# Performance work log

Hardware: AMD Instinct MI355X
Metric: run time of the kernel (lower is better)

Reference implementation:

```python
import jax, jax.numpy as jnp
import numpy as np

T, D, I, E, K = 256, 2048, 5632, 8, 2
P = (I * D + 4) // 5  # TQ1_0: 5 ternary values per byte
_MULT = (1, 3, 9, 27, 81)


def _unpack_tq10(packed, out_dim, in_dim):
    # packed: int32 [P], each value is a base-3 byte encoding 5 ternary digits
    digits = jnp.stack([(packed // m) % 3 for m in _MULT], axis=1)  # [P,5]
    w = digits.reshape(-1)[: out_dim * in_dim] - 1  # {-1,0,+1}
    return w.reshape(out_dim, in_dim).astype(jnp.float32)


def _tmm(x, w_packed, s, out_dim, in_dim):
    # ternary_matmul_direct: dequant ternary weight, per-output-row scale
    w = _unpack_tq10(w_packed, out_dim, in_dim)  # [out,in]
    return (x @ w.T) * s.reshape(1, -1)


def setup_inputs() -> dict:
    key = jax.random.key(0)
    ks = jax.random.split(key, 16)
    inp = {}
    inp["x"] = jax.random.normal(ks[0], (T, D), jnp.float32)
    inp["router_w"] = jax.random.normal(ks[1], (E, D), jnp.float32) * 0.02
    inp["gate_packed"] = jax.random.randint(ks[2], (E, P), 0, 243, jnp.int32)
    inp["up_packed"] = jax.random.randint(ks[3], (E, P), 0, 243, jnp.int32)
    inp["down_packed"] = jax.random.randint(ks[4], (E, P), 0, 243, jnp.int32)
    inp["gate_s"] = jax.random.uniform(ks[5], (E, I, 1), jnp.float32, 0.01, 0.05)
    inp["up_s"] = jax.random.uniform(ks[6], (E, I, 1), jnp.float32, 0.01, 0.05)
    inp["down_s"] = jax.random.uniform(ks[7], (E, D, 1), jnp.float32, 0.01, 0.05)
    inp["sh_gate_w"] = jax.random.randint(ks[8], (I, D), -127, 128, jnp.int32)
    inp["sh_up_w"] = jax.random.randint(ks[9], (I, D), -127, 128, jnp.int32)
    inp["sh_down_w"] = jax.random.randint(ks[10], (D, I), -127, 128, jnp.int32)
    inp["sh_gate_s"] = jax.random.uniform(ks[11], (I, 1), jnp.float32, 0.005, 0.02)
    inp["sh_up_s"] = jax.random.uniform(ks[12], (I, 1), jnp.float32, 0.005, 0.02)
    inp["sh_down_s"] = jax.random.uniform(ks[13], (D, 1), jnp.float32, 0.005, 0.02)
    return inp


def reference(x, router_w, gate_packed, up_packed, down_packed,
              gate_s, up_s, down_s,
              sh_gate_w, sh_up_w, sh_down_w,
              sh_gate_s, sh_up_s, sh_down_s):
    n_tok = x.shape[0]
    # ---- router: top-k + softmax over selected logits -> dense gate matrix [T,E]
    logits = x @ router_w.T
    topv, topi = jax.lax.top_k(logits, K)
    probs = jax.nn.softmax(topv, axis=-1)
    gates = jnp.zeros((n_tok, E), x.dtype).at[jnp.arange(n_tok)[:, None], topi].add(probs)
    # ---- shared INT8 SwiGLU expert (dequant matmul, per-row fp scale)
    g = jax.nn.silu((x @ sh_gate_w.T.astype(jnp.float32)) * sh_gate_s.reshape(1, -1))
    u = (x @ sh_up_w.T.astype(jnp.float32)) * sh_up_s.reshape(1, -1)
    out = ((g * u) @ sh_down_w.T.astype(jnp.float32)) * sh_down_s.reshape(1, -1)
    # ---- routed ternary TQ1_0 experts (unpack -> dequant -> SwiGLU)
    for e in range(E):
        ge = jax.nn.silu(_tmm(x, gate_packed[e], gate_s[e], I, D))
        ue = _tmm(x, up_packed[e], up_s[e], I, D)
        ye = _tmm(ge * ue, down_packed[e], down_s[e], D, I)
        out = out + gates[:, e:e + 1] * ye
    return out
```

## Files before the change

kernel.cpp:

```cpp
#include <hip/hip_runtime.h>
#include <hip/hip_bf16.h>
#include <stdint.h>

#define TT 256
#define DD 2048
#define II 5632
#define EE 8
#define PP 2306868

typedef __attribute__((ext_vector_type(8))) short bf16x8;
typedef __attribute__((ext_vector_type(4))) float f32x4;
typedef unsigned int uint;

__device__ __forceinline__ ushort f2b_rne(float f) {
  __hip_bfloat16 h = __float2bfloat16(f);
  return __builtin_bit_cast(ushort, h);
}

__device__ __forceinline__ uint pk_bf16(float lo, float hi) {
  uint r;
  asm("v_cvt_pk_bf16_f32 %0, %1, %2" : "=v"(r) : "v"(lo), "v"(hi));
  return r;
}

__device__ __forceinline__ bf16x8 ld_a(const ushort* p) {
  uint4 v = *(const uint4*)p;
  return __builtin_bit_cast(bf16x8, v);
}

__device__ __forceinline__ bf16x8 tern_frag(const int* __restrict__ pk, uint i0, uint ph) {
  uint p0 = (uint)pk[i0], p1 = (uint)pk[i0 + 1], p2 = (uint)pk[i0 + 2];
  uint P = p0 + 243u * p1 + 59049u * p2;
  uint c1 = P / 3u, c2 = c1 / 3u, c3 = c2 / 3u, c4 = c3 / 3u;
  uint Q = ph == 0 ? P : (ph == 1 ? c1 : (ph == 2 ? c2 : (ph == 3 ? c3 : c4)));
  uint w0, w1, w2, w3;
#define DIGPAIR(wout) { uint qa = Q / 3u; float flo = (float)(int)(Q - 3u * qa) - 1.0f; \
    uint qb = qa / 3u; float fhi = (float)(int)(qa - 3u * qb) - 1.0f; Q = qb;          \
    wout = pk_bf16(flo, fhi); }
  DIGPAIR(w0) DIGPAIR(w1) DIGPAIR(w2) DIGPAIR(w3)
#undef DIGPAIR
  uint4 u = make_uint4(w0, w1, w2, w3);
  return __builtin_bit_cast(bf16x8, u);
}

__device__ __forceinline__ bf16x8 i8_frag(const int* __restrict__ w, long off) {
  int4 a = *(const int4*)(w + off);
  int4 b = *(const int4*)(w + off + 4);
  uint4 u;
  u.x = pk_bf16((float)a.x, (float)a.y);
  u.y = pk_bf16((float)a.z, (float)a.w);
  u.z = pk_bf16((float)b.x, (float)b.y);
  u.w = pk_bf16((float)b.z, (float)b.w);
  return __builtin_bit_cast(bf16x8, u);
}

__global__ __launch_bounds__(64) void k_router(const float* __restrict__ x,
                                               const float* __restrict__ rw,
                                               int* __restrict__ cnt,
                                               int* __restrict__ tok,
                                               float* __restrict__ tokg,
                                               ushort* __restrict__ xb) {
  const int t = blockIdx.x;
  const int lane = threadIdx.x;
  const float* xp = x + (long)t * DD;
  ushort* xbp = xb + (long)t * DD;
#pragma unroll
  for (int it = 0; it < DD / (64 * 8); ++it) {
    int d = lane * 8 + it * 512;
    float4 a = *(const float4*)(xp + d);
    float4 b = *(const float4*)(xp + d + 4);
    ushort o[8];
    o[0] = f2b_rne(a.x); o[1] = f2b_rne(a.y); o[2] = f2b_rne(a.z); o[3] = f2b_rne(a.w);
    o[4] = f2b_rne(b.x); o[5] = f2b_rne(b.y); o[6] = f2b_rne(b.z); o[7] = f2b_rne(b.w);
    *(uint4*)(xbp + d) = *(uint4*)&o[0];
  }
  float lg[EE];
#pragma unroll
  for (int e = 0; e < EE; ++e) {
    const float* wp = rw + e * DD;
    float acc = 0.f;
    for (int d = lane; d < DD; d += 64) acc += xp[d] * wp[d];
#pragma unroll
    for (int off = 32; off > 0; off >>= 1) acc += __shfl_down(acc, off, 64);
    lg[e] = acc;
  }
  if (lane == 0) {
    int e1 = 0; float v1 = lg[0];
#pragma unroll
    for (int e = 1; e < EE; ++e) if (lg[e] > v1) { v1 = lg[e]; e1 = e; }
    int e2 = -1; float v2 = -3.4e38f;
#pragma unroll
    for (int e = 0; e < EE; ++e) if (e != e1 && lg[e] > v2) { v2 = lg[e]; e2 = e; }
    float ex2 = __expf(v2 - v1);
    float inv = 1.f / (1.f + ex2);
    int s1 = atomicAdd(&cnt[e1], 1);
    tok[e1 * TT + s1] = t; tokg[e1 * TT + s1] = inv;
    int s2 = atomicAdd(&cnt[e2], 1);
    tok[e2 * TT + s2] = t; tokg[e2 * TT + s2] = ex2 * inv;
  }
}

__global__ __launch_bounds__(256) void k_gateup_all(const ushort* __restrict__ xb,
                                                    const int* __restrict__ cnt,
                                                    const int* __restrict__ tok,
                                                    const int* __restrict__ gate_p,
                                                    const int* __restrict__ up_p,
                                                    const float* __restrict__ gate_s,
                                                    const float* __restrict__ up_s,
                                                    const int* __restrict__ shg,
                                                    const int* __restrict__ shu,
                                                    const float* __restrict__ shg_s,
                                                    const float* __restrict__ shu_s,
                                                    ushort* __restrict__ hsh,
                                                    ushort* __restrict__ hrt) {
  const int n0 = blockIdx.x * 64;
  const int tid = threadIdx.x;
  const int lane = tid & 63, wid = tid >> 6;
  const int col = lane & 15, kg8 = (lane >> 4) * 8;
  const int n_lane = n0 + wid * 16 + col;
  const int z = blockIdx.z;

  if (z == 8) {
    if (blockIdx.y >= 2) return;
    const int m0 = blockIdx.y * 128;
    const long nd = (long)n_lane * DD;
    f32x4 ag[8], au[8];
#pragma unroll
    for (int m = 0; m < 8; ++m) { ag[m] = {0.f,0.f,0.f,0.f}; au[m] = {0.f,0.f,0.f,0.f}; }
#pragma unroll 1
    for (int kt = 0; kt < DD / 64; ++kt) {
#pragma unroll
      for (int kh = 0; kh < 2; ++kh) {
        const int kf = kt * 64 + kh * 32 + kg8;
        bf16x8 bg = i8_frag(shg, nd + kf);
        bf16x8 bu = i8_frag(shu, nd + kf);
#pragma unroll
        for (int m = 0; m < 8; ++m) {
          bf16x8 av = ld_a(xb + (long)(m0 + m * 16 + col) * DD + kf);
          ag[m] = __builtin_amdgcn_mfma_f32_16x16x32_bf16(av, bg, ag[m], 0, 0, 0);
          au[m] = __builtin_amdgcn_mfma_f32_16x16x32_bf16(av, bu, au[m], 0, 0, 0);
        }
      }
    }
    const float sg = shg_s[n_lane];
    const float su = shu_s[n_lane];
#pragma unroll
    for (int m = 0; m < 8; ++m)
#pragma unroll
      for (int i = 0; i < 4; ++i) {
        int mr = m0 + m * 16 + (lane >> 4) * 4 + i;
        float g = ag[m][i] * sg, u = au[m][i] * su;
        float h = g / (1.f + __expf(-g)) * u;
        hsh[(long)mr * II + n_lane] = f2b_rne(h);
      }
  } else {
    const int e = z;
    const int ne = cnt[e];
    const int m0 = blockIdx.y * 64;
    if (m0 >= ne) return;
    long arow[4];
#pragma unroll
    for (int m = 0; m < 4; ++m) {
      int s = m0 + m * 16 + col;
      if (s >= ne) s = ne - 1;
      arow[m] = (long)tok[e * TT + s] * DD;
    }
    const int* gp = gate_p + (long)e * PP;
    const int* up = up_p + (long)e * PP;
    const uint nd = (uint)n_lane * DD;
    f32x4 ag[4], au[4];
#pragma unroll
    for (int m = 0; m < 4; ++m) { ag[m] = {0.f,0.f,0.f,0.f}; au[m] = {0.f,0.f,0.f,0.f}; }
#pragma unroll 1
    for (int kt = 0; kt < DD / 64; ++kt) {
#pragma unroll
      for (int kh = 0; kh < 2; ++kh) {
        const int kf = kt * 64 + kh * 32 + kg8;
        const uint q = nd + (uint)kf;
        const uint i0 = q / 5u;
        const uint ph = q - 5u * i0;
        bf16x8 bg = tern_frag(gp, i0, ph);
        bf16x8 bu = tern_frag(up, i0, ph);
#pragma unroll
        for (int m = 0; m < 4; ++m) {
          bf16x8 av = ld_a(xb + arow[m] + kf);
          ag[m] = __builtin_amdgcn_mfma_f32_16x16x32_bf16(av, bg, ag[m], 0, 0, 0);
          au[m] = __builtin_amdgcn_mfma_f32_16x16x32_bf16(av, bu, au[m], 0, 0, 0);
        }
      }
    }
    const float sg = gate_s[(long)e * II + n_lane];
    const float su = up_s[(long)e * II + n_lane];
    ushort* hb = hrt + (long)e * TT * II;
#pragma unroll
    for (int m = 0; m < 4; ++m)
#pragma unroll
      for (int i = 0; i < 4; ++i) {
        int mr = m0 + m * 16 + (lane >> 4) * 4 + i;
        float g = ag[m][i] * sg, u = au[m][i] * su;
        float h = g / (1.f + __expf(-g)) * u;
        hb[(long)mr * II + n_lane] = f2b_rne(h);
      }
  }
}

__global__ __launch_bounds__(256) void k_down_all(const ushort* __restrict__ hsh,
                                                  const ushort* __restrict__ hrt,
                                                  const int* __restrict__ down_p,
                                                  const float* __restrict__ down_s,
                                                  const int* __restrict__ shd,
                                                  const float* __restrict__ shd_s,
                                                  const int* __restrict__ cnt,
                                                  const int* __restrict__ tok,
                                                  const float* __restrict__ tokg,
                                                  float* __restrict__ out) {
  const int n0 = blockIdx.x * 64;
  const int tid = threadIdx.x;
  const int lane = tid & 63, wid = tid >> 6;
  const int col = lane & 15, kg8 = (lane >> 4) * 8;
  const int n_lane = n0 + wid * 16 + col;
  const int z = blockIdx.z;

  if (z >= 16) {
    if (blockIdx.y >= 2) return;
    const int ks = z - 16;
    const int m0 = blockIdx.y * 128;
    const long nd = (long)n_lane * II;
    f32x4 acc[8];
#pragma unroll
    for (int m = 0; m < 8; ++m) acc[m] = {0.f,0.f,0.f,0.f};
#pragma unroll 1
    for (int kt = ks * 22; kt < ks * 22 + 22; ++kt) {
#pragma unroll
      for (int kh = 0; kh < 2; ++kh) {
        const int kf = kt * 64 + kh * 32 + kg8;
        bf16x8 bv = i8_frag(shd, nd + kf);
#pragma unroll
        for (int m = 0; m < 8; ++m) {
          bf16x8 av = ld_a(hsh + (long)(m0 + m * 16 + col) * II + kf);
          acc[m] = __builtin_amdgcn_mfma_f32_16x16x32_bf16(av, bv, acc[m], 0, 0, 0);
        }
      }
    }
    const float sd = shd_s[n_lane];
#pragma unroll
    for (int m = 0; m < 8; ++m)
#pragma unroll
      for (int i = 0; i < 4; ++i) {
        int mr = m0 + m * 16 + (lane >> 4) * 4 + i;
        atomicAdd(&out[(long)mr * DD + n_lane], acc[m][i] * sd);
      }
  } else {
    const int e = z >> 1, ks = z & 1;
    const int ne = cnt[e];
    const int m0 = blockIdx.y * 64;
    if (m0 >= ne) return;
    const int* dp = down_p + (long)e * PP;
    const ushort* abase = hrt + (long)(e * TT + m0 + col) * II;
    const uint nd = (uint)n_lane * II;
    f32x4 acc[4];
#pragma unroll
    for (int m = 0; m < 4; ++m) acc[m] = {0.f,0.f,0.f,0.f};
#pragma unroll 1
    for (int kt = ks * 44; kt < ks * 44 + 44; ++kt) {
#pragma unroll
      for (int kh = 0; kh < 2; ++kh) {
        const int kf = kt * 64 + kh * 32 + kg8;
        const uint q = nd + (uint)kf;
        const uint i0 = q / 5u;
        const uint ph = q - 5u * i0;
        bf16x8 bv = tern_frag(dp, i0, ph);
#pragma unroll
        for (int m = 0; m < 4; ++m) {
          bf16x8 av = ld_a(abase + (long)m * 16 * II + kf);
          acc[m] = __builtin_amdgcn_mfma_f32_16x16x32_bf16(av, bv, acc[m], 0, 0, 0);
        }
      }
    }
    const float sd = down_s[(long)e * DD + n_lane];
#pragma unroll
    for (int m = 0; m < 4; ++m)
#pragma unroll
      for (int i = 0; i < 4; ++i) {
        int mr = m0 + m * 16 + (lane >> 4) * 4 + i;
        if (mr < ne) {
          float v = acc[m][i] * sd * tokg[e * TT + mr];
          atomicAdd(&out[(long)tok[e * TT + mr] * DD + n_lane], v);
        }
      }
  }
}

extern "C" void kernel_launch(void* const* d_in, const int* in_sizes, int n_in,
                              void* d_out, int out_size, void* d_ws, size_t ws_size,
                              hipStream_t stream) {
  const float* x        = (const float*)d_in[0];
  const float* router_w = (const float*)d_in[1];
  const int*   gate_p   = (const int*)d_in[2];
  const int*   up_p     = (const int*)d_in[3];
  const int*   down_p   = (const int*)d_in[4];
  const float* gate_s   = (const float*)d_in[5];
  const float* up_s     = (const float*)d_in[6];
  const float* down_s   = (const float*)d_in[7];
  const int*   shg      = (const int*)d_in[8];
  const int*   shu      = (const int*)d_in[9];
  const int*   shd      = (const int*)d_in[10];
  const float* shg_s    = (const float*)d_in[11];
  const float* shu_s    = (const float*)d_in[12];
  const float* shd_s    = (const float*)d_in[13];
  float* out = (float*)d_out;

  char* ws = (char*)d_ws;
  int*    cnt  = (int*)ws;
  int*    tok  = (int*)(ws + 1024);
  float*  tokg = (float*)(ws + 9216);
  ushort* xb   = (ushort*)(ws + 32768);
  ushort* hsh  = (ushort*)(ws + 32768 + 1048576);
  ushort* hrt  = (ushort*)(ws + 32768 + 1048576 + 2883584);

  hipMemsetAsync(cnt, 0, 64, stream);
  hipMemsetAsync(out, 0, (size_t)TT * DD * 4, stream);
  k_router<<<TT, 64, 0, stream>>>(x, router_w, cnt, tok, tokg, xb);
  k_gateup_all<<<dim3(88, 4, 9), 256, 0, stream>>>(xb, cnt, tok, gate_p, up_p, gate_s, up_s,
                                                   shg, shu, shg_s, shu_s, hsh, hrt);
  k_down_all<<<dim3(32, 4, 20), 256, 0, stream>>>(hsh, hrt, down_p, down_s, shd, shd_s,
                                                  cnt, tok, tokg, out);
}
```

Baseline: 1.000 ms.

## Stage ternary and int8 weight chunks through LDS with coalesced loads

Weights for the gate/up and down projections are now loaded cooperatively into shared memory per K-chunk. Ternary packed words go in as int4 rows, and int8 weights are converted to bf16 and stored with an XOR swizzle. MFMA B fragments are then read from LDS instead of through scattered per-lane global loads, aiming to coalesce weight traffic and cut redundant or unaligned global reads. The cost is an extra pair of __syncthreads per chunk with no double buffering, plus added LDS usage that may lower occupancy.

```diff
diff --git a/kernel.cpp b/kernel.cpp
--- a/kernel.cpp
+++ b/kernel.cpp
@@ -28,8 +28,7 @@
   return __builtin_bit_cast(bf16x8, v);
 }
 
-__device__ __forceinline__ bf16x8 tern_frag(const int* __restrict__ pk, uint i0, uint ph) {
-  uint p0 = (uint)pk[i0], p1 = (uint)pk[i0 + 1], p2 = (uint)pk[i0 + 2];
+__device__ __forceinline__ bf16x8 tern_digits(uint p0, uint p1, uint p2, uint ph) {
   uint P = p0 + 243u * p1 + 59049u * p2;
   uint c1 = P / 3u, c2 = c1 / 3u, c3 = c2 / 3u, c4 = c3 / 3u;
   uint Q = ph == 0 ? P : (ph == 1 ? c1 : (ph == 2 ? c2 : (ph == 3 ? c3 : c4)));
@@ -43,15 +42,47 @@
   return __builtin_bit_cast(bf16x8, u);
 }
 
-__device__ __forceinline__ bf16x8 i8_frag(const int* __restrict__ w, long off) {
-  int4 a = *(const int4*)(w + off);
-  int4 b = *(const int4*)(w + off + 4);
-  uint4 u;
-  u.x = pk_bf16((float)a.x, (float)a.y);
-  u.y = pk_bf16((float)a.z, (float)a.w);
-  u.z = pk_bf16((float)b.x, (float)b.y);
-  u.w = pk_bf16((float)b.z, (float)b.w);
-  return __builtin_bit_cast(bf16x8, u);
+__device__ __forceinline__ void stage_tern_chunk(const int* __restrict__ pk,
+                                                 int n0, int din, int c0,
+                                                 int* lw, int tid) {
+  const int j = tid & 15;
+  if (j < 14) {
+#pragma unroll
+    for (int it = 0; it < 4; ++it) {
+      int r = it * 16 + (tid >> 4);
+      uint q0 = (uint)(n0 + r) * (uint)din + (uint)c0;
+      uint a = (q0 / 5u) & ~3u;
+      uint idx = a + (uint)(j * 4);
+      if (idx > (uint)(PP - 4)) idx = (uint)(PP - 4);
+      int4 v = *(const int4*)(pk + idx);
+      *(int4*)&lw[r * 60 + j * 4] = v;
+    }
+  }
+}
+
+__device__ __forceinline__ void stage_i8_chunk(const int* __restrict__ w,
+                                               int n0, int din, int c0,
+                                               ushort* lb, int tid) {
+  const int lane = tid & 63, wid = tid >> 6;
+#pragma unroll
+  for (int it = 0; it < 8; ++it) {
+    int r = it * 8 + wid * 2 + (lane >> 5);
+    int jj = (lane & 31) * 4;
+    int4 v = *(const int4*)(w + (long)(n0 + r) * din + c0 + jj);
+    uint2 o;
+    o.x = pk_bf16((float)v.x, (float)v.y);
+    o.y = pk_bf16((float)v.z, (float)v.w);
+    uint byte = (uint)(r * 256 + jj * 2);
+    byte ^= (uint)((r & 7) << 4);
+    *(uint2*)((char*)lb + byte) = o;
+  }
+}
+
+__device__ __forceinline__ bf16x8 ld_b_sw(const ushort* lb, int row, int klocal) {
+  uint byte = (uint)(row * 256 + klocal * 2);
+  byte ^= (uint)((row & 7) << 4);
+  uint4 v = *(const uint4*)((const char*)lb + byte);
+  return __builtin_bit_cast(bf16x8, v);
 }
 
 __global__ __launch_bounds__(64) void k_router(const float* __restrict__ x,
@@ -113,27 +144,35 @@
                                                     const float* __restrict__ shu_s,
                                                     ushort* __restrict__ hsh,
                                                     ushort* __restrict__ hrt) {
+  __shared__ __align__(16) char smem[32768];
   const int n0 = blockIdx.x * 64;
   const int tid = threadIdx.x;
   const int lane = tid & 63, wid = tid >> 6;
   const int col = lane & 15, kg8 = (lane >> 4) * 8;
-  const int n_lane = n0 + wid * 16 + col;
+  const int lrow = wid * 16 + col;
+  const int n_lane = n0 + lrow;
   const int z = blockIdx.z;
 
   if (z == 8) {
     if (blockIdx.y >= 2) return;
     const int m0 = blockIdx.y * 128;
-    const long nd = (long)n_lane * DD;
+    ushort* lbg = (ushort*)smem;
+    ushort* lbu = lbg + 64 * 128;
     f32x4 ag[8], au[8];
 #pragma unroll
     for (int m = 0; m < 8; ++m) { ag[m] = {0.f,0.f,0.f,0.f}; au[m] = {0.f,0.f,0.f,0.f}; }
 #pragma unroll 1
-    for (int kt = 0; kt < DD / 64; ++kt) {
-#pragma unroll
-      for (int kh = 0; kh < 2; ++kh) {
-        const int kf = kt * 64 + kh * 32 + kg8;
-        bf16x8 bg = i8_frag(shg, nd + kf);
-        bf16x8 bu = i8_frag(shu, nd + kf);
+    for (int c = 0; c < 16; ++c) {
+      __syncthreads();
+      stage_i8_chunk(shg, n0, DD, c * 128, lbg, tid);
+      stage_i8_chunk(shu, n0, DD, c * 128, lbu, tid);
+      __syncthreads();
+#pragma unroll
+      for (int kk = 0; kk < 4; ++kk) {
+        const int klocal = kk * 32 + kg8;
+        bf16x8 bg = ld_b_sw(lbg, lrow, klocal);
+        bf16x8 bu = ld_b_sw(lbu, lrow, klocal);
+        const int kf = c * 128 + klocal;
 #pragma unroll
         for (int m = 0; m < 8; ++m) {
           bf16x8 av = ld_a(xb + (long)(m0 + m * 16 + col) * DD + kf);
@@ -165,22 +204,31 @@
       if (s >= ne) s = ne - 1;
       arow[m] = (long)tok[e * TT + s] * DD;
     }
+    int* lwg = (int*)smem;
+    int* lwu = lwg + 64 * 60;
     const int* gp = gate_p + (long)e * PP;
     const int* up = up_p + (long)e * PP;
-    const uint nd = (uint)n_lane * DD;
+    const uint nb = (uint)n_lane * DD;
     f32x4 ag[4], au[4];
 #pragma unroll
     for (int m = 0; m < 4; ++m) { ag[m] = {0.f,0.f,0.f,0.f}; au[m] = {0.f,0.f,0.f,0.f}; }
 #pragma unroll 1
-    for (int kt = 0; kt < DD / 64; ++kt) {
-#pragma unroll
-      for (int kh = 0; kh < 2; ++kh) {
-        const int kf = kt * 64 + kh * 32 + kg8;
-        const uint q = nd + (uint)kf;
+    for (int c = 0; c < 8; ++c) {
+      __syncthreads();
+      stage_tern_chunk(gp, n0, DD, c * 256, lwg, tid);
+      stage_tern_chunk(up, n0, DD, c * 256, lwu, tid);
+      __syncthreads();
+      const uint a = ((nb + (uint)(c * 256)) / 5u) & ~3u;
+#pragma unroll 2
+      for (int kk = 0; kk < 8; ++kk) {
+        const int kf = c * 256 + kk * 32 + kg8;
+        const uint q = nb + (uint)kf;
         const uint i0 = q / 5u;
         const uint ph = q - 5u * i0;
-        bf16x8 bg = tern_frag(gp, i0, ph);
-        bf16x8 bu = tern_frag(up, i0, ph);
+        const int* pg = lwg + lrow * 60 + (int)(i0 - a);
+        const int* pu = lwu + lrow * 60 + (int)(i0 - a);
+        bf16x8 bg = tern_digits((uint)pg[0], (uint)pg[1], (uint)pg[2], ph);
+        bf16x8 bu = tern_digits((uint)pu[0], (uint)pu[1], (uint)pu[2], ph);
 #pragma unroll
         for (int m = 0; m < 4; ++m) {
           bf16x8 av = ld_a(xb + arow[m] + kf);
@@ -214,27 +262,34 @@
                                                   const int* __restrict__ tok,
                                                   const float* __restrict__ tokg,
                                                   float* __restrict__ out) {
+  __shared__ __align__(16) char smem[16384];
   const int n0 = blockIdx.x * 64;
   const int tid = threadIdx.x;
   const int lane = tid & 63, wid = tid >> 6;
   const int col = lane & 15, kg8 = (lane >> 4) * 8;
-  const int n_lane = n0 + wid * 16 + col;
+  const int lrow = wid * 16 + col;
+  const int n_lane = n0 + lrow;
   const int z = blockIdx.z;
 
   if (z >= 16) {
     if (blockIdx.y >= 2) return;
     const int ks = z - 16;
     const int m0 = blockIdx.y * 128;
-    const long nd = (long)n_lane * II;
+    ushort* lb = (ushort*)smem;
     f32x4 acc[8];
 #pragma unroll
     for (int m = 0; m < 8; ++m) acc[m] = {0.f,0.f,0.f,0.f};
 #pragma unroll 1
-    for (int kt = ks * 22; kt < ks * 22 + 22; ++kt) {
-#pragma unroll
-      for (int kh = 0; kh < 2; ++kh) {
-        const int kf = kt * 64 + kh * 32 + kg8;
-        bf16x8 bv = i8_frag(shd, nd + kf);
+    for (int cc = 0; cc < 11; ++cc) {
+      const int c = ks * 11 + cc;
+      __syncthreads();
+      stage_i8_chunk(shd, n0, II, c * 128, lb, tid);
+      __syncthreads();
+#pragma unroll
+      for (int kk = 0; kk < 4; ++kk) {
+        const int klocal = kk * 32 + kg8;
+        bf16x8 bv = ld_b_sw(lb, lrow, klocal);
+        const int kf = c * 128 + klocal;
 #pragma unroll
         for (int m = 0; m < 8; ++m) {
           bf16x8 av = ld_a(hsh + (long)(m0 + m * 16 + col) * II + kf);
@@ -255,21 +310,28 @@
     const int ne = cnt[e];
     const int m0 = blockIdx.y * 64;
     if (m0 >= ne) return;
+    int* lw = (int*)smem;
     const int* dp = down_p + (long)e * PP;
     const ushort* abase = hrt + (long)(e * TT + m0 + col) * II;
-    const uint nd = (uint)n_lane * II;
+    const uint nb = (uint)n_lane * II;
     f32x4 acc[4];
 #pragma unroll
     for (int m = 0; m < 4; ++m) acc[m] = {0.f,0.f,0.f,0.f};
 #pragma unroll 1
-    for (int kt = ks * 44; kt < ks * 44 + 44; ++kt) {
-#pragma unroll
-      for (int kh = 0; kh < 2; ++kh) {
-        const int kf = kt * 64 + kh * 32 + kg8;
-        const uint q = nd + (uint)kf;
+    for (int cc = 0; cc < 11; ++cc) {
+      const int c = ks * 11 + cc;
+      __syncthreads();
+      stage_tern_chunk(dp, n0, II, c * 256, lw, tid);
+      __syncthreads();
+      const uint a = ((nb + (uint)(c * 256)) / 5u) & ~3u;
+#pragma unroll 2
+      for (int kk = 0; kk < 8; ++kk) {
+        const int kf = c * 256 + kk * 32 + kg8;
+        const uint q = nb + (uint)kf;
         const uint i0 = q / 5u;
         const uint ph = q - 5u * i0;
-        bf16x8 bv = tern_frag(dp, i0, ph);
+        const int* p = lw + lrow * 60 + (int)(i0 - a);
+        bf16x8 bv = tern_digits((uint)p[0], (uint)p[1], (uint)p[2], ph);
 #pragma unroll
         for (int m = 0; m < 4; ++m) {
           bf16x8 av = ld_a(abase + (long)m * 16 * II + kf);
```

New measurement: 971.0 us. -2.9%, faster.
